# Optimization experiments

Measured on AMD Instinct MI355X. Metric: run time of the kernel, lower is better.

## Reference

```python
import jax, jax.numpy as jnp
import numpy as np

VOCAB, EMBED, HID, LAYERS, NGRAPH = 50000, 128, 256, 3, 128

def setup_inputs() -> dict:
    key = jax.random.key(0)
    ks = jax.random.split(key, 16)
    N, E = 50000, 800000
    x_lex = jax.random.randint(ks[0], (N,), 0, VOCAB)
    edge_index = jax.random.randint(ks[1], (2, E), 0, N)
    batch = jnp.sort(jax.random.randint(ks[2], (N,), 0, NGRAPH))
    s = lambda k, shp, fan: jax.random.normal(k, shp, jnp.float32) * (1.0 / np.sqrt(fan))
    return {
        "x_lex": x_lex, "edge_index": edge_index, "batch": batch,
        "embed_table": s(ks[3], (VOCAB, EMBED), EMBED),
        "W_proj": s(ks[4], (HID, EMBED), EMBED),                 # F.linear random-projection branch
        "ggnn_weight": s(ks[5], (LAYERS, HID, HID), HID),        # per-layer message transform
        "W_ih": s(ks[6], (3 * HID, HID), HID), "b_ih": jnp.zeros((3 * HID,), jnp.float32),
        "W_hh": s(ks[7], (3 * HID, HID), HID), "b_hh": jnp.zeros((3 * HID,), jnp.float32),
        "W1": s(ks[8], (HID // 4, HID), HID), "b1": jnp.zeros((HID // 4,), jnp.float32),
        "W2": s(ks[9], (1, HID // 4), HID // 4), "b2": jnp.zeros((1,), jnp.float32),
    }

def _gru_cell(a, h, W_ih, b_ih, W_hh, b_hh):
    gi = a @ W_ih.T + b_ih   # [N, 3H]
    gh = h @ W_hh.T + b_hh
    i_r, i_z, i_n = jnp.split(gi, 3, axis=-1)
    h_r, h_z, h_n = jnp.split(gh, 3, axis=-1)
    r = jax.nn.sigmoid(i_r + h_r)
    z = jax.nn.sigmoid(i_z + h_z)
    n = jnp.tanh(i_n + r * h_n)
    return (1.0 - z) * n + z * h

def reference(x_lex, edge_index, batch, embed_table, W_proj, ggnn_weight,
              W_ih, b_ih, W_hh, b_hh, W1, b1, W2, b2):
    N = x_lex.shape[0]
    x = embed_table[x_lex]                 # [N, EMBED]
    x = x @ W_proj.T                       # project to HID (embed_dim != hidden_dim branch)
    src, dst = edge_index[0], edge_index[1]
    h = x
    for i in range(LAYERS):
        m = h @ ggnn_weight[i]             # [N, HID] per-layer linear
        agg = jax.ops.segment_sum(m[src], dst, num_segments=N)  # scatter-add aggregation
        h = _gru_cell(agg, h, W_ih, b_ih, W_hh, b_hh)
    h_pool = jax.ops.segment_max(h, batch, num_segments=NGRAPH)  # global_max_pool [G, HID]
    logits = jax.nn.relu(h_pool @ W1.T + b1) @ W2.T + b2          # [G, 1]
    return (logits, h_pool)
```

## Files before the change

### kernel.cpp

```cpp
#include <hip/hip_runtime.h>
#include <math.h>

constexpr int HID = 256;

typedef __attribute__((ext_vector_type(8))) short bf16x8;
typedef __attribute__((ext_vector_type(4))) float f32x4;

__device__ __forceinline__ float bf2f(unsigned short u){
    union { unsigned int i; float f; } v; v.i = ((unsigned int)u) << 16; return v.f;
}
__device__ __forceinline__ unsigned short f2bf(float f){
    union { float f; unsigned int i; } v; v.f = f;
    return (unsigned short)((v.i + 0x7fffu + ((v.i >> 16) & 1u)) >> 16);
}
__device__ __forceinline__ float sigm(float x){ return 1.f / (1.f + __expf(-x)); }

__device__ __forceinline__ int xcd_chunk(int bid, int nwg){
    int q = nwg >> 3, r = nwg & 7;
    int xcd = bid & 7, pos = bid >> 3;
    return (xcd < r) ? xcd * (q + 1) + pos : r * (q + 1) + (xcd - r) * q + pos;
}

__device__ __forceinline__ void gll16(const unsigned short* g, unsigned short* l){
    __builtin_amdgcn_global_load_lds(
        (const __attribute__((address_space(1))) void*)g,
        (__attribute__((address_space(3))) void*)l, 16, 0, 0);
}

__global__ void k_prep(const float* __restrict__ Wproj, const float* __restrict__ Wih,
                       const float* __restrict__ Whh, const float* __restrict__ Wg,
                       const float* __restrict__ embed, const int* __restrict__ idx,
                       const int* __restrict__ edst, int E, int* __restrict__ deg,
                       unsigned short* __restrict__ wproj, unsigned short* __restrict__ wih,
                       unsigned short* __restrict__ whh, unsigned short* __restrict__ wg,
                       unsigned short* __restrict__ x0, int Nn, int EMB){
    const long n1 = (long)HID * EMB, n2 = 3L * HID * HID;
    const long n5 = (long)Nn * EMB;
    const long tot = n1 + 3 * n2 + n5 + E;
    for (long i = blockIdx.x * (long)blockDim.x + threadIdx.x; i < tot;
         i += (long)gridDim.x * blockDim.x){
        long j = i;
        if (j < n1){ wproj[j] = f2bf(Wproj[j]); continue; }
        j -= n1;
        if (j < n2){ wih[j] = f2bf(Wih[j]); continue; }
        j -= n2;
        if (j < n2){ whh[j] = f2bf(Whh[j]); continue; }
        j -= n2;
        if (j < n2){ wg[j] = f2bf(Wg[j]); continue; }
        j -= n2;
        if (j < n5){
            int row = (int)(j / EMB), k = (int)(j % EMB);
            x0[j] = f2bf(embed[(size_t)idx[row] * EMB + k]);
            continue;
        }
        j -= n5;
        atomicAdd(&deg[edst[j]], 1);
    }
}

__global__ void k_scanA(const int* __restrict__ deg, int N, int* __restrict__ bsum){
    __shared__ int red[512];
    int b = blockIdx.x, tid = threadIdx.x;
    int i = b * 512 + tid;
    red[tid] = (i < N) ? deg[i] : 0;
    __syncthreads();
    for (int o = 256; o > 0; o >>= 1){
        if (tid < o) red[tid] += red[tid + o];
        __syncthreads();
    }
    if (tid == 0) bsum[b] = red[0];
}

__global__ void k_scanB(int* __restrict__ bsum, int nb){
    __shared__ int s[1024];
    int tid = threadIdx.x;
    s[tid] = (tid < nb) ? bsum[tid] : 0;
    __syncthreads();
    for (int o = 1; o < 1024; o <<= 1){
        int v = (tid >= o) ? s[tid - o] : 0;
        __syncthreads();
        s[tid] += v;
        __syncthreads();
    }
    if (tid < nb) bsum[tid] = (tid > 0) ? s[tid - 1] : 0;
    if (tid == nb) bsum[nb] = s[nb - 1];
}

__global__ void k_scanC(const int* __restrict__ deg, int N, const int* __restrict__ bsum,
                        int* __restrict__ off){
    __shared__ int s[512];
    int b = blockIdx.x, tid = threadIdx.x;
    int i = b * 512 + tid;
    int v = (i < N) ? deg[i] : 0;
    s[tid] = v;
    __syncthreads();
    for (int o = 1; o < 512; o <<= 1){
        int t = (tid >= o) ? s[tid - o] : 0;
        __syncthreads();
        s[tid] += t;
        __syncthreads();
    }
    int ex = bsum[b] + ((tid > 0) ? s[tid - 1] : 0);
    if (i < N) off[i] = ex;
    else if (i == N) off[N] = ex;
}

__global__ void k_fill(const int* __restrict__ src, const int* __restrict__ dst, int E,
                       const int* __restrict__ off, int* __restrict__ cursor,
                       int* __restrict__ csr_src){
    int i = blockIdx.x*blockDim.x + threadIdx.x;
    if (i < E){
        int d = dst[i];
        int p = off[d] + atomicAdd(&cursor[d], 1);
        csr_src[p] = src[i];
    }
}

__global__ void k_agg(const unsigned short* __restrict__ h, const int* __restrict__ off,
                      const int* __restrict__ csr, unsigned short* __restrict__ out, int N){
    int wave = threadIdx.x >> 6, lane = threadIdx.x & 63;
    int d = blockIdx.x * 8 + wave * 2 + (lane >> 5);
    if (d >= N) return;
    int c = (lane & 31) * 8;
    float a[8] = {};
    int s0 = off[d], s1 = off[d + 1];
    int j = s0;
    for (; j + 3 < s1; j += 4){
        int sA = csr[j], sB = csr[j + 1], sC = csr[j + 2], sD = csr[j + 3];
        bf16x8 vA = *(const bf16x8*)(h + (size_t)sA * HID + c);
        bf16x8 vB = *(const bf16x8*)(h + (size_t)sB * HID + c);
        bf16x8 vC = *(const bf16x8*)(h + (size_t)sC * HID + c);
        bf16x8 vD = *(const bf16x8*)(h + (size_t)sD * HID + c);
        #pragma unroll
        for (int q = 0; q < 8; q++)
            a[q] += (bf2f((unsigned short)vA[q]) + bf2f((unsigned short)vB[q]))
                  + (bf2f((unsigned short)vC[q]) + bf2f((unsigned short)vD[q]));
    }
    for (; j < s1; j++){
        bf16x8 vA = *(const bf16x8*)(h + (size_t)csr[j] * HID + c);
        #pragma unroll
        for (int q = 0; q < 8; q++) a[q] += bf2f((unsigned short)vA[q]);
    }
    bf16x8 o;
    #pragma unroll
    for (int q = 0; q < 8; q++) o[q] = (short)f2bf(a[q]);
    *(bf16x8*)(out + (size_t)d * HID + c) = o;
}

__global__ __launch_bounds__(256, 3) void k_mmS(
    const unsigned short* __restrict__ A, const unsigned short* __restrict__ B,
    unsigned short* __restrict__ C, int M, int N, int K,
    int nbx, long lsB, long lsC)
{
    __shared__ __align__(16) unsigned short sm[3 * 1024 * 8];
    const int tid = threadIdx.x, w = tid >> 6, l = tid & 63;
    const int wm = w >> 1, wn = w & 1, lr = l & 15, lk = l >> 4;

    const int orig = xcd_chunk(blockIdx.x, gridDim.x);
    const int layer = orig / nbx, sub = orig % nbx;
    B += layer * lsB;
    C += layer * lsC;
    const int nby = N >> 7;
    const long row0 = (long)(sub / nby) * 128;
    const int  col0 = (sub % nby) * 128;

    long aoff0, aoff1, boff0, boff1;
    {
        int r0 = tid >> 2,          kc0 = tid & 3;
        int r1 = (tid + 256) >> 2,  kc1 = tid & 3;
        long g0 = row0 + r0; if (g0 > M - 1) g0 = M - 1;
        long g1 = row0 + r1; if (g1 > M - 1) g1 = M - 1;
        aoff0 = g0 * (long)K + (kc0 ^ ((r0 >> 1) & 3)) * 8;
        aoff1 = g1 * (long)K + (kc1 ^ ((r1 >> 1) & 3)) * 8;
        boff0 = (long)(col0 + r0) * K + (kc0 ^ ((r0 >> 1) & 3)) * 8;
        boff1 = (long)(col0 + r1) * K + (kc1 ^ ((r1 >> 1) & 3)) * 8;
    }
    auto STAGE = [&](int T, int buf){
        const int ka = T * 32;
        unsigned short* d = sm + (size_t)buf * 8192;
        gll16(A + aoff0 + ka, d + (0 * 256 + w * 64) * 8);
        gll16(A + aoff1 + ka, d + (1 * 256 + w * 64) * 8);
        gll16(B + boff0 + ka, d + (2 * 256 + w * 64) * 8);
        gll16(B + boff1 + ka, d + (3 * 256 + w * 64) * 8);
    };

    int raddrA[4], raddrB[4];
    #pragma unroll
    for (int i = 0; i < 4; i++){
        int ra = wm * 64 + i * 16 + lr;
        raddrA[i] = (ra * 4 + (lk ^ ((ra >> 1) & 3))) * 8;
        int rb = wn * 64 + i * 16 + lr;
        raddrB[i] = (512 + rb * 4 + (lk ^ ((rb >> 1) & 3))) * 8;
    }

    const int NT = K >> 5;
    STAGE(0, 0);
    STAGE(1, 1);

    f32x4 acc[4][4] = {};
    for (int t = 0; t < NT; t++){
        if (t < NT - 1) asm volatile("s_waitcnt vmcnt(4)" ::: "memory");
        else            asm volatile("s_waitcnt vmcnt(0)" ::: "memory");
        __builtin_amdgcn_s_barrier();
        if (t + 2 < NT) STAGE(t + 2, (t + 2) % 3);

        const unsigned short* bufp = sm + (size_t)(t % 3) * 8192;
        bf16x8 af[4], bfb[4];
        #pragma unroll
        for (int i = 0; i < 4; i++){
            af[i]  = *(const bf16x8*)(bufp + raddrA[i]);
            bfb[i] = *(const bf16x8*)(bufp + raddrB[i]);
        }
        __builtin_amdgcn_s_setprio(1);
        #pragma unroll
        for (int mi = 0; mi < 4; mi++)
            #pragma unroll
            for (int ni = 0; ni < 4; ni++)
                acc[mi][ni] = __builtin_amdgcn_mfma_f32_16x16x32_bf16(af[mi], bfb[ni], acc[mi][ni], 0, 0, 0);
        __builtin_amdgcn_s_setprio(0);
    }

    #pragma unroll
    for (int mi = 0; mi < 4; mi++)
        #pragma unroll
        for (int ni = 0; ni < 4; ni++)
            #pragma unroll
            for (int r = 0; r < 4; r++){
                long row = row0 + wm * 64 + mi * 16 + lk * 4 + r;
                if (row < M){
                    int col = col0 + wn * 64 + ni * 16 + lr;
                    C[row * (long)N + col] = f2bf(acc[mi][ni][r]);
                }
            }
}

__global__ __launch_bounds__(256, 3) void k_gru(
    const unsigned short* __restrict__ AGG, const unsigned short* __restrict__ H,
    const unsigned short* __restrict__ WE, const unsigned short* __restrict__ WH,
    const float* __restrict__ bih, const float* __restrict__ bhh,
    unsigned short* __restrict__ HN, int M)
{
    __shared__ __align__(16) unsigned short sm[3 * 1024 * 8];
    const int tid = threadIdx.x, w = tid >> 6, l = tid & 63;
    const int wm = w >> 1, wn = w & 1, lr = l & 15, lk = l >> 4;
    const int orig = xcd_chunk(blockIdx.x, gridDim.x);
    const long row0 = (long)(orig >> 2) * 64;
    const int  c0 = (orig & 3) * 64;

    long aoff, boff[3];
    {
        int r0 = tid >> 2, kc = tid & 3;
        long g0 = row0 + r0; if (g0 > M - 1) g0 = M - 1;
        int sw = (kc ^ ((r0 >> 1) & 3)) * 8;
        aoff = g0 * HID + sw;
        #pragma unroll
        for (int q = 0; q < 3; q++)
            boff[q] = (long)(q * HID + c0 + r0) * HID + sw;
    }
    auto STAGE = [&](int T, int buf){
        const unsigned short* As = (T < 8) ? AGG : H;
        const unsigned short* Bs = (T < 8) ? WE  : WH;
        const int ka = (T & 7) * 32;
        unsigned short* d = sm + (size_t)buf * 8192;
        gll16(As + aoff + ka, d + (w * 64) * 8);
        #pragma unroll
        for (int q = 0; q < 3; q++)
            gll16(Bs + boff[q] + ka, d + (256 + q * 256 + w * 64) * 8);
    };

    int raddrA[2], raddrB[3][2];
    #pragma unroll
    for (int i = 0; i < 2; i++){
        int ra = wm * 32 + i * 16 + lr;
        raddrA[i] = (ra * 4 + (lk ^ ((ra >> 1) & 3))) * 8;
    }
    #pragma unroll
    for (int j = 0; j < 3; j++)
        #pragma unroll
        for (int ni = 0; ni < 2; ni++){
            int rb = wn * 32 + ni * 16 + lr;
            raddrB[j][ni] = (256 + j * 256 + rb * 4 + (lk ^ ((rb >> 1) & 3))) * 8;
        }

    f32x4 aR[2][2] = {}, aZ[2][2] = {}, aI[2][2] = {}, aHn[2][2] = {};

    STAGE(0, 0);
    STAGE(1, 1);

    #pragma unroll
    for (int t = 0; t < 16; t++){
        if (t < 15) asm volatile("s_waitcnt vmcnt(4)" ::: "memory");
        else        asm volatile("s_waitcnt vmcnt(0)" ::: "memory");
        __builtin_amdgcn_s_barrier();
        if (t + 2 < 16) STAGE(t + 2, (t + 2) % 3);

        const unsigned short* bufp = sm + (size_t)(t % 3) * 8192;
        bf16x8 a[2], bb[3][2];
        #pragma unroll
        for (int i = 0; i < 2; i++) a[i] = *(const bf16x8*)(bufp + raddrA[i]);
        #pragma unroll
        for (int j = 0; j < 3; j++)
            #pragma unroll
            for (int ni = 0; ni < 2; ni++)
                bb[j][ni] = *(const bf16x8*)(bufp + raddrB[j][ni]);

        __builtin_amdgcn_s_setprio(1);
        #pragma unroll
        for (int ni = 0; ni < 2; ni++)
            #pragma unroll
            for (int mi = 0; mi < 2; mi++){
                aR[mi][ni] = __builtin_amdgcn_mfma_f32_16x16x32_bf16(a[mi], bb[0][ni], aR[mi][ni], 0, 0, 0);
                aZ[mi][ni] = __builtin_amdgcn_mfma_f32_16x16x32_bf16(a[mi], bb[1][ni], aZ[mi][ni], 0, 0, 0);
                if (t < 8)
                    aI[mi][ni]  = __builtin_amdgcn_mfma_f32_16x16x32_bf16(a[mi], bb[2][ni], aI[mi][ni], 0, 0, 0);
                else
                    aHn[mi][ni] = __builtin_amdgcn_mfma_f32_16x16x32_bf16(a[mi], bb[2][ni], aHn[mi][ni], 0, 0, 0);
            }
        __builtin_amdgcn_s_setprio(0);
    }

    #pragma unroll
    for (int ni = 0; ni < 2; ni++){
        int gc = c0 + wn * 32 + ni * 16 + lr;
        float br  = bih[gc] + bhh[gc];
        float bz  = bih[HID + gc] + bhh[HID + gc];
        float bin = bih[2 * HID + gc];
        float bhn = bhh[2 * HID + gc];
        #pragma unroll
        for (int mi = 0; mi < 2; mi++)
            #pragma unroll
            for (int r = 0; r < 4; r++){
                long row = row0 + wm * 32 + mi * 16 + lk * 4 + r;
                if (row < M){
                    float rr = sigm(aR[mi][ni][r] + br);
                    float zz = sigm(aZ[mi][ni][r] + bz);
                    float nn = tanhf(aI[mi][ni][r] + bin + rr * (aHn[mi][ni][r] + bhn));
                    float hv = bf2f(H[row * HID + gc]);
                    HN[row * HID + gc] = f2bf((1.f - zz) * nn + zz * hv);
                }
            }
    }
}

__global__ void k_pool_mlp(const unsigned short* __restrict__ h, const int* __restrict__ batch,
                           int Nn, int G,
                           const float* __restrict__ W1, const float* __restrict__ b1,
                           const float* __restrict__ W2, const float* __restrict__ b2,
                           float* __restrict__ out){
    int g = blockIdx.x;
    __shared__ float pool[HID];
    __shared__ float hid[64];

    int lo = 0, hi = Nn;
    while (lo < hi){ int mid = (lo + hi) >> 1; if (batch[mid] < g) lo = mid + 1; else hi = mid; }
    int s = lo;
    lo = s; hi = Nn;
    while (lo < hi){ int mid = (lo + hi) >> 1; if (batch[mid] < g + 1) lo = mid + 1; else hi = mid; }
    int e = lo;

    int c = threadIdx.x;
    float mx = -INFINITY;
    for (int i = s; i < e; i++) mx = fmaxf(mx, bf2f(h[(size_t)i * HID + c]));
    pool[c] = mx;
    out[(size_t)G + (size_t)g * HID + c] = mx;
    __syncthreads();

    if (c < 64){
        float sacc = b1[c];
        for (int k = 0; k < HID; k++) sacc += pool[k] * W1[c * HID + k];
        hid[c] = fmaxf(sacc, 0.f) * W2[c];
    }
    __syncthreads();
    if (c == 0){
        float sacc = b2[0];
        for (int j = 0; j < 64; j++) sacc += hid[j];
        out[g] = sacc;
    }
}

extern "C" void kernel_launch(void* const* d_in, const int* in_sizes, int n_in,
                              void* d_out, int out_size, void* d_ws, size_t ws_size,
                              hipStream_t stream){
    const int*   x_lex = (const int*)d_in[0];
    const int*   edge  = (const int*)d_in[1];
    const int*   batch = (const int*)d_in[2];
    const float* embed = (const float*)d_in[3];
    const float* Wproj = (const float*)d_in[4];
    const float* Wg    = (const float*)d_in[5];
    const float* Wih   = (const float*)d_in[6];
    const float* bih   = (const float*)d_in[7];
    const float* Whh   = (const float*)d_in[8];
    const float* bhh   = (const float*)d_in[9];
    const float* W1    = (const float*)d_in[10];
    const float* b1    = (const float*)d_in[11];
    const float* W2    = (const float*)d_in[12];
    const float* b2    = (const float*)d_in[13];

    int Nn  = in_sizes[0];
    int E   = in_sizes[1] / 2;
    int G   = out_size / (1 + HID);
    int EMB = in_sizes[4] / HID;

    const int* esrc = edge;
    const int* edst = edge + E;

    size_t HH = (size_t)HID * HID;
    unsigned short* x0    = (unsigned short*)d_ws;
    unsigned short* hA    = x0    + (size_t)Nn * EMB;
    unsigned short* hB    = hA    + (size_t)Nn * HID;
    unsigned short* aggh  = hB    + (size_t)Nn * HID;
    unsigned short* wproj = aggh  + (size_t)Nn * HID;
    unsigned short* wih   = wproj + (size_t)HID * EMB;
    unsigned short* whh   = wih   + 3 * HH;
    unsigned short* wg    = whh   + 3 * HH;
    unsigned short* weff  = wg    + 3 * HH;
    int* deg    = (int*)(weff + 9 * HH);
    int* cursor = deg + Nn;
    int* off    = cursor + Nn;
    int* csr    = off + Nn + 1;
    int nbScan  = (Nn + 511) / 512;
    int* bsum   = csr + E;

    size_t ush = (size_t)Nn * (EMB + 3 * HID) + (size_t)HID * EMB + 18 * HH;
    size_t needed = ush * 2 + (size_t)(3 * Nn + 2 + E + nbScan + 1) * sizeof(int);
    if (ws_size < needed) return;

    hipMemsetAsync(deg, 0, sizeof(int) * (size_t)(2 * Nn), stream);
    k_prep<<<2048, 256, 0, stream>>>(Wproj, Wih, Whh, Wg, embed, x_lex,
                                     edst, E, deg,
                                     wproj, wih, whh, wg, x0, Nn, EMB);
    k_scanA<<<nbScan, 512, 0, stream>>>(deg, Nn, bsum);
    k_scanB<<<1, 1024, 0, stream>>>(bsum, nbScan);
    k_scanC<<<(Nn + 512) / 512, 512, 0, stream>>>(deg, Nn, bsum, off);
    k_fill <<<(E + 255) / 256, 256, 0, stream>>>(esrc, edst, E, off, cursor, csr);

    k_mmS<<<36, 256, 0, stream>>>(wih, wg, weff, 3 * HID, HID, HID,
                                  12, (long)HH, (long)(3 * HH));

    int mb = (Nn + 127) / 128;

    k_mmS<<<mb * 2, 256, 0, stream>>>(x0, wproj, hA, Nn, HID, EMB,
                                      mb * 2, 0L, 0L);

    int gruBlocks = ((Nn + 63) / 64) * 4;

    unsigned short* hc = hA;
    unsigned short* hn = hB;
    for (int lay = 0; lay < 3; lay++){
        k_agg<<<(Nn + 7) / 8, 256, 0, stream>>>(hc, off, csr, aggh, Nn);
        k_gru<<<gruBlocks, 256, 0, stream>>>(
            aggh, hc, weff + (size_t)lay * 3 * HH, whh, bih, bhh, hn, Nn);
        unsigned short* t = hc; hc = hn; hn = t;
    }

    k_pool_mlp<<<G, HID, 0, stream>>>(hc, batch, Nn, G, W1, b1, W2, b2, (float*)d_out);
}
```

Measured before the change: 588.8 us.

## Load GRU A fragments directly to registers and double-buffer weights via LDS

The GRU GEMM kernel no longer stages the activation tile through LDS. Each wave loads its A fragments straight from global memory into registers. Only the weight tiles go through LDS, now with register staging and a two-buffer scheme in place of the three-buffer global_load_lds pipeline. This shrinks shared memory use and raises the launch-bounds occupancy target from 3 to 6, aiming for more concurrent blocks. The cost is a second barrier per k-step, register-staged stores, and non-coalesced 16-byte A loads that may expose global latency.

```diff
diff --git a/kernel.cpp b/kernel.cpp
--- a/kernel.cpp
+++ b/kernel.cpp
@@ -234,70 +234,71 @@
             }
 }
 
-__global__ __launch_bounds__(256, 3) void k_gru(
+__global__ __launch_bounds__(256, 6) void k_gru(
     const unsigned short* __restrict__ AGG, const unsigned short* __restrict__ H,
     const unsigned short* __restrict__ WE, const unsigned short* __restrict__ WH,
     const float* __restrict__ bih, const float* __restrict__ bhh,
     unsigned short* __restrict__ HN, int M)
 {
-    __shared__ __align__(16) unsigned short sm[3 * 1024 * 8];
+    __shared__ __align__(16) unsigned short sm[2 * 3 * 256 * 8];
     const int tid = threadIdx.x, w = tid >> 6, l = tid & 63;
     const int wm = w >> 1, wn = w & 1, lr = l & 15, lk = l >> 4;
     const int orig = xcd_chunk(blockIdx.x, gridDim.x);
     const long row0 = (long)(orig >> 2) * 64;
     const int  c0 = (orig & 3) * 64;
 
-    long aoff, boff[3];
-    {
-        int r0 = tid >> 2, kc = tid & 3;
-        long g0 = row0 + r0; if (g0 > M - 1) g0 = M - 1;
-        int sw = (kc ^ ((r0 >> 1) & 3)) * 8;
-        aoff = g0 * HID + sw;
-        #pragma unroll
-        for (int q = 0; q < 3; q++)
-            boff[q] = (long)(q * HID + c0 + r0) * HID + sw;
-    }
-    auto STAGE = [&](int T, int buf){
-        const unsigned short* As = (T < 8) ? AGG : H;
-        const unsigned short* Bs = (T < 8) ? WE  : WH;
-        const int ka = (T & 7) * 32;
-        unsigned short* d = sm + (size_t)buf * 8192;
-        gll16(As + aoff + ka, d + (w * 64) * 8);
-        #pragma unroll
-        for (int q = 0; q < 3; q++)
-            gll16(Bs + boff[q] + ka, d + (256 + q * 256 + w * 64) * 8);
-    };
-
-    int raddrA[2], raddrB[3][2];
-    #pragma unroll
-    for (int i = 0; i < 2; i++){
-        int ra = wm * 32 + i * 16 + lr;
-        raddrA[i] = (ra * 4 + (lk ^ ((ra >> 1) & 3))) * 8;
-    }
+    const int r0 = tid >> 2, kc = tid & 3;
+    const int wslot = r0 * 4 + (kc ^ ((r0 >> 1) & 3));
+    long bgoff[3];
+    #pragma unroll
+    for (int q = 0; q < 3; q++)
+        bgoff[q] = (long)(q * HID + c0 + r0) * HID + kc * 8;
+
+    long agoff[2];
+    #pragma unroll
+    for (int mi = 0; mi < 2; mi++){
+        long row = row0 + wm * 32 + mi * 16 + lr;
+        if (row > M - 1) row = M - 1;
+        agoff[mi] = row * HID + lk * 8;
+    }
+
+    int raddrB[3][2];
     #pragma unroll
     for (int j = 0; j < 3; j++)
         #pragma unroll
         for (int ni = 0; ni < 2; ni++){
             int rb = wn * 32 + ni * 16 + lr;
-            raddrB[j][ni] = (256 + j * 256 + rb * 4 + (lk ^ ((rb >> 1) & 3))) * 8;
+            raddrB[j][ni] = (j * 256 + rb * 4 + (lk ^ ((rb >> 1) & 3))) * 8;
         }
 
     f32x4 aR[2][2] = {}, aZ[2][2] = {}, aI[2][2] = {}, aHn[2][2] = {};
-
-    STAGE(0, 0);
-    STAGE(1, 1);
+    bf16x8 aA[2][2], bR[3];
+
+    #pragma unroll
+    for (int q = 0; q < 3; q++) bR[q] = *(const bf16x8*)(WE + bgoff[q]);
+    #pragma unroll
+    for (int mi = 0; mi < 2; mi++) aA[0][mi] = *(const bf16x8*)(AGG + agoff[mi]);
+    #pragma unroll
+    for (int q = 0; q < 3; q++) *(bf16x8*)(sm + (size_t)(q * 256 + wslot) * 8) = bR[q];
 
     #pragma unroll
     for (int t = 0; t < 16; t++){
-        if (t < 15) asm volatile("s_waitcnt vmcnt(4)" ::: "memory");
-        else        asm volatile("s_waitcnt vmcnt(0)" ::: "memory");
+        asm volatile("s_waitcnt lgkmcnt(0)" ::: "memory");
         __builtin_amdgcn_s_barrier();
-        if (t + 2 < 16) STAGE(t + 2, (t + 2) % 3);
-
-        const unsigned short* bufp = sm + (size_t)(t % 3) * 8192;
-        bf16x8 a[2], bb[3][2];
-        #pragma unroll
-        for (int i = 0; i < 2; i++) a[i] = *(const bf16x8*)(bufp + raddrA[i]);
+
+        if (t + 1 < 16){
+            const unsigned short* Wn = (t + 1 < 8) ? WE : WH;
+            const unsigned short* An = (t + 1 < 8) ? AGG : H;
+            const int ka = ((t + 1) & 7) * 32;
+            #pragma unroll
+            for (int q = 0; q < 3; q++) bR[q] = *(const bf16x8*)(Wn + bgoff[q] + ka);
+            #pragma unroll
+            for (int mi = 0; mi < 2; mi++)
+                aA[(t + 1) & 1][mi] = *(const bf16x8*)(An + agoff[mi] + ka);
+        }
+
+        const unsigned short* bufp = sm + (size_t)(t & 1) * 6144;
+        bf16x8 bb[3][2];
         #pragma unroll
         for (int j = 0; j < 3; j++)
             #pragma unroll
@@ -309,14 +310,23 @@
         for (int ni = 0; ni < 2; ni++)
             #pragma unroll
             for (int mi = 0; mi < 2; mi++){
-                aR[mi][ni] = __builtin_amdgcn_mfma_f32_16x16x32_bf16(a[mi], bb[0][ni], aR[mi][ni], 0, 0, 0);
-                aZ[mi][ni] = __builtin_amdgcn_mfma_f32_16x16x32_bf16(a[mi], bb[1][ni], aZ[mi][ni], 0, 0, 0);
+                aR[mi][ni] = __builtin_amdgcn_mfma_f32_16x16x32_bf16(aA[t & 1][mi], bb[0][ni], aR[mi][ni], 0, 0, 0);
+                aZ[mi][ni] = __builtin_amdgcn_mfma_f32_16x16x32_bf16(aA[t & 1][mi], bb[1][ni], aZ[mi][ni], 0, 0, 0);
                 if (t < 8)
-                    aI[mi][ni]  = __builtin_amdgcn_mfma_f32_16x16x32_bf16(a[mi], bb[2][ni], aI[mi][ni], 0, 0, 0);
+                    aI[mi][ni]  = __builtin_amdgcn_mfma_f32_16x16x32_bf16(aA[t & 1][mi], bb[2][ni], aI[mi][ni], 0, 0, 0);
                 else
-                    aHn[mi][ni] = __builtin_amdgcn_mfma_f32_16x16x32_bf16(a[mi], bb[2][ni], aHn[mi][ni], 0, 0, 0);
+                    aHn[mi][ni] = __builtin_amdgcn_mfma_f32_16x16x32_bf16(aA[t & 1][mi], bb[2][ni], aHn[mi][ni], 0, 0, 0);
             }
         __builtin_amdgcn_s_setprio(0);
+
+        asm volatile("s_waitcnt lgkmcnt(0)" ::: "memory");
+        __builtin_amdgcn_s_barrier();
+
+        if (t + 1 < 16){
+            unsigned short* d = sm + (size_t)((t + 1) & 1) * 6144;
+            #pragma unroll
+            for (int q = 0; q < 3; q++) *(bf16x8*)(d + (size_t)(q * 256 + wslot) * 8) = bR[q];
+        }
     }
 
     #pragma unroll
```

After: 2.242 ms. 281% more time.
